# Performance work log

Measured on AMD Instinct MI355X. Metric: run time of the kernel, lower is better.

The kernel has to match this reference:

```python
import jax, jax.numpy as jnp
import numpy as np

IN_F = 256
OUT_F = 256
HYPER = 128
BATCH = 4096


def setup_inputs() -> dict:
    key = jax.random.key(0)
    ks = jax.random.split(key, 9)
    s_in = 1.0 / np.sqrt(IN_F)
    s_h = 1.0 / np.sqrt(HYPER)
    x = jax.random.normal(ks[0], (BATCH, IN_F), dtype=jnp.float32)
    # weight_gen: Linear(in, hyper) -> ReLU -> Linear(hyper, in*out)
    W1g = jax.random.uniform(ks[1], (IN_F, HYPER), jnp.float32, -s_in, s_in)
    b1g = jax.random.uniform(ks[2], (HYPER,), jnp.float32, -s_in, s_in)
    W2g = jax.random.uniform(ks[3], (HYPER, IN_F * OUT_F), jnp.float32, -s_h, s_h)
    b2g = jax.random.uniform(ks[4], (IN_F * OUT_F,), jnp.float32, -s_h, s_h)
    # bias_gen: Linear(in, hyper) -> ReLU -> Linear(hyper, out)
    W1b = jax.random.uniform(ks[5], (IN_F, HYPER), jnp.float32, -s_in, s_in)
    b1b = jax.random.uniform(ks[6], (HYPER,), jnp.float32, -s_in, s_in)
    W2b = jax.random.uniform(ks[7], (HYPER, OUT_F), jnp.float32, -s_h, s_h)
    b2b = jax.random.uniform(ks[8], (OUT_F,), jnp.float32, -s_h, s_h)
    return {"x": x, "W1g": W1g, "b1g": b1g, "W2g": W2g, "b2g": b2g,
            "W1b": W1b, "b1b": b1b, "W2b": W2b, "b2b": b2b}


def reference(x, W1g, b1g, W2g, b2g, W1b, b1b, W2b, b2b):
    B = x.shape[0]
    # generate per-sample weights [B, out, in]
    hg = jax.nn.relu(x @ W1g + b1g)                      # [B, hyper]
    weights = (hg @ W2g + b2g).reshape(B, OUT_F, IN_F)   # [B, out, in]
    # generate per-sample bias [B, out]
    hb = jax.nn.relu(x @ W1b + b1b)                      # [B, hyper]
    bias = hb @ W2b + b2b                                # [B, out]
    # batched matvec: bmm(weights, x[...,None]) + bias
    out = jnp.einsum('boi,bi->bo', weights, x) + bias    # [B, out]
    return out
```

## Files before the change

kernel.cpp:

```cpp
#include <hip/hip_runtime.h>

#define AS1 __attribute__((address_space(1)))
#define AS3 __attribute__((address_space(3)))

typedef short short8 __attribute__((ext_vector_type(8)));
typedef float f32x16 __attribute__((ext_vector_type(16)));
typedef unsigned short ushort4v __attribute__((ext_vector_type(4)));

#define BATCH 4096
#define IN_F 256
#define OUT_F 256
#define HYP 128
#define HX 129
#define KP (HX * IN_F)
#define NBUILD (OUT_F * HX / 8)

__device__ __forceinline__ float bf2f(unsigned short u) {
  unsigned v = ((unsigned)u) << 16;
  float f;
  __builtin_memcpy(&f, &v, 4);
  return f;
}
__device__ __forceinline__ unsigned short f2bf(float f) {
  unsigned u;
  __builtin_memcpy(&u, &f, 4);
  unsigned r = u + 0x7fffu + ((u >> 16) & 1u);
  return (unsigned short)(r >> 16);
}

__device__ __forceinline__ void gld_lds16(const unsigned short* g, unsigned short* s) {
  __builtin_amdgcn_global_load_lds((const AS1 unsigned int*)g, (AS3 unsigned int*)s, 16, 0, 0);
}

__global__ __launch_bounds__(256) void k_prep(
    const float* __restrict__ x,
    const float* __restrict__ W1g, const float* __restrict__ b1g,
    const float* __restrict__ W2g, const float* __restrict__ b2g,
    const float* __restrict__ W1b, const float* __restrict__ b1b,
    const float* __restrict__ W2b, const float* __restrict__ b2b,
    unsigned short* __restrict__ Vb,
    unsigned short* __restrict__ hgbT,
    unsigned short* __restrict__ xb,
    float* __restrict__ out) {
  __shared__ float xl[16 * IN_F];
  __shared__ float hbl[16 * HYP];
  __shared__ unsigned short hgt[HYP * 16];
  const int t = threadIdx.x;

  if (blockIdx.x >= 256) {
    const int cid = (blockIdx.x - 256) * 256 + t;
    const int ic = cid & 31;
    const int pair = cid >> 5;
    const int h = pair % HX;
    const int o = pair / HX;
    const float* src = (h < HYP) ? (W2g + (size_t)h * (OUT_F * IN_F) + o * IN_F + ic * 8)
                                 : (b2g + o * IN_F + ic * 8);
    const float4 v0 = ((const float4*)src)[0];
    const float4 v1 = ((const float4*)src)[1];
    uint4 pk;
    pk.x = (unsigned)f2bf(v0.x) | ((unsigned)f2bf(v0.y) << 16);
    pk.y = (unsigned)f2bf(v0.z) | ((unsigned)f2bf(v0.w) << 16);
    pk.z = (unsigned)f2bf(v1.x) | ((unsigned)f2bf(v1.y) << 16);
    pk.w = (unsigned)f2bf(v1.z) | ((unsigned)f2bf(v1.w) << 16);
    *(uint4*)(Vb + (size_t)o * KP + h * IN_F + ic * 8) = pk;
    return;
  }

  const int r0 = blockIdx.x * 16;
  for (int j0 = 0; j0 < 16 * IN_F; j0 += 256) {
    const float v = x[(size_t)r0 * IN_F + j0 + t];
    xl[j0 + t] = v;
    xb[(size_t)r0 * IN_F + j0 + t] = f2bf(v);
  }
  __syncthreads();
  const int h = t & 127;
  const int rb = (t >> 7) * 8;
  float ag[8] = {0.f, 0.f, 0.f, 0.f, 0.f, 0.f, 0.f, 0.f};
  float av[8] = {0.f, 0.f, 0.f, 0.f, 0.f, 0.f, 0.f, 0.f};
  for (int i = 0; i < IN_F; ++i) {
    const float wg = W1g[i * HYP + h];
    const float wb = W1b[i * HYP + h];
#pragma unroll
    for (int r = 0; r < 8; ++r) {
      const float xv = xl[(rb + r) * IN_F + i];
      ag[r] += xv * wg;
      av[r] += xv * wb;
    }
  }
  const float bg = b1g[h], bb = b1b[h];
#pragma unroll
  for (int r = 0; r < 8; ++r) {
    float g = ag[r] + bg; g = g > 0.f ? g : 0.f;
    float v = av[r] + bb; v = v > 0.f ? v : 0.f;
    hgt[h * 16 + rb + r] = f2bf(g);
    hbl[(rb + r) * HYP + h] = v;
  }
  __syncthreads();
  {
    const int h2 = t >> 1, part = t & 1;
    const uint4 pk = *(const uint4*)&hgt[h2 * 16 + part * 8];
    *(uint4*)&hgbT[(size_t)h2 * BATCH + r0 + part * 8] = pk;
  }
  float acc[16];
#pragma unroll
  for (int r = 0; r < 16; ++r) acc[r] = 0.f;
  for (int hh = 0; hh < HYP; ++hh) {
    const float w = W2b[hh * OUT_F + t];
#pragma unroll
    for (int r = 0; r < 16; ++r) acc[r] += hbl[r * HYP + hh] * w;
  }
  const float bo = b2b[t];
#pragma unroll
  for (int r = 0; r < 16; ++r) out[(size_t)(r0 + r) * OUT_F + t] = acc[r] + bo;
}

__global__ __launch_bounds__(512, 2) void k_gemm(const unsigned short* __restrict__ Vb,
                                                 const unsigned short* __restrict__ hgbT,
                                                 const unsigned short* __restrict__ xb,
                                                 float* __restrict__ out) {
  __shared__ __align__(16) unsigned short Bl[2][64 * 256];
  __shared__ __align__(16) unsigned short hgs[33 * 256];
  const int tid = threadIdx.x;
  const int lane = tid & 63;
  const int wave = tid >> 6;
  const int l31 = lane & 31;
  const int hi = lane >> 5;
  const int wm = wave & 3;
  const int wo = wave >> 2;

  const int bid = blockIdx.x;
  const int c = bid & 7;
  const int t2 = bid >> 3;
  const int xm = t2 & 15;
  const int g8 = t2 >> 4;
  const int grp = c + 8 * g8;
  const int yo = grp & 3;
  const int z = grp >> 2;

  const int m0 = xm * 256;
  const int o0 = yo * 64;
  const int hBeg = (z * HX) >> 2;
  const int hEnd = ((z + 1) * HX) >> 2;
  const int nh = hEnd - hBeg;

  for (int idx = tid; idx < nh * 256; idx += 512) {
    const int hl = idx >> 8;
    const int hh = hBeg + hl;
    hgs[idx] = (hh == HYP) ? (unsigned short)0x3F80
                           : hgbT[(size_t)hh * BATCH + m0 + (idx & 255)];
  }

  const int mrow0 = m0 + wm * 64 + l31;
  const int mrow1 = mrow0 + 32;
  uint4 xf0[16], xf1[16];
#pragma unroll
  for (int j = 0; j < 16; ++j) {
    xf0[j] = *(const uint4*)(xb + (size_t)mrow0 * IN_F + j * 16 + hi * 8);
    xf1[j] = *(const uint4*)(xb + (size_t)mrow1 * IN_F + j * 16 + hi * 8);
  }

  const int nB = tid >> 5;
  const int p = tid & 31;
  const int cs = p ^ (nB & 7);
  const unsigned short* gsrc = Vb + (size_t)(o0 + nB) * KP + cs * 8 + (size_t)hBeg * IN_F;

  f32x16 zv;
#pragma unroll
  for (int i = 0; i < 16; ++i) zv[i] = 0.0f;
  f32x16 acc0 = zv, acc1 = zv;
  f32x16 ah0 = zv, ah1 = zv;

#pragma unroll
  for (int j = 0; j < 4; ++j)
    gld_lds16(gsrc + (size_t)j * 16 * KP, &Bl[0][(tid + 512 * j) * 8]);
  __syncthreads();

  for (int r = 0; r < nh; ++r) {
    const int buf = r & 1;
    if (r + 1 < nh) {
      const unsigned short* gs = gsrc + (size_t)(r + 1) * IN_F;
#pragma unroll
      for (int j = 0; j < 4; ++j)
        gld_lds16(gs + (size_t)j * 16 * KP, &Bl[buf ^ 1][(tid + 512 * j) * 8]);
    }
    const unsigned short* bp = &Bl[buf][0];
    const int rowb = wo * 32 + l31;
#pragma unroll
    for (int ic = 0; ic < 4; ++ic) {
#pragma unroll
      for (int t = 0; t < 4; ++t) {
        const int c0 = ic * 8 + t * 2 + hi;
        const int pr = c0 ^ (l31 & 7);
        const short8 b0 = *(const short8*)(bp + rowb * 256 + pr * 8);
        const short8 a0 = __builtin_bit_cast(short8, xf0[ic * 4 + t]);
        const short8 a1 = __builtin_bit_cast(short8, xf1[ic * 4 + t]);
        ah0 = __builtin_amdgcn_mfma_f32_32x32x16_bf16(a0, b0, ah0, 0, 0, 0);
        ah1 = __builtin_amdgcn_mfma_f32_32x32x16_bf16(a1, b0, ah1, 0, 0, 0);
      }
    }
#pragma unroll
    for (int q = 0; q < 4; ++q) {
      const ushort4v v0 = *(const ushort4v*)&hgs[r * 256 + wm * 64 + 4 * hi + q * 8];
      const ushort4v v1 = *(const ushort4v*)&hgs[r * 256 + wm * 64 + 32 + 4 * hi + q * 8];
#pragma unroll
      for (int e = 0; e < 4; ++e) {
        acc0[q * 4 + e] += bf2f(v0[e]) * ah0[q * 4 + e];
        acc1[q * 4 + e] += bf2f(v1[e]) * ah1[q * 4 + e];
      }
    }
    ah0 = zv; ah1 = zv;
    __syncthreads();
  }

  const int mb = m0 + wm * 64 + 4 * hi;
  const int col = o0 + wo * 32 + l31;
#pragma unroll
  for (int g = 0; g < 16; ++g) {
    const int row0 = mb + (g & 3) + 8 * (g >> 2);
    atomicAdd(&out[(size_t)row0 * OUT_F + col], acc0[g]);
    atomicAdd(&out[(size_t)(row0 + 32) * OUT_F + col], acc1[g]);
  }
}

extern "C" void kernel_launch(void* const* d_in, const int* in_sizes, int n_in,
                              void* d_out, int out_size, void* d_ws, size_t ws_size,
                              hipStream_t stream) {
  const float* x = (const float*)d_in[0];
  const float* W1g = (const float*)d_in[1];
  const float* b1g = (const float*)d_in[2];
  const float* W2g = (const float*)d_in[3];
  const float* b2g = (const float*)d_in[4];
  const float* W1b = (const float*)d_in[5];
  const float* b1b = (const float*)d_in[6];
  const float* W2b = (const float*)d_in[7];
  const float* b2b = (const float*)d_in[8];
  float* out = (float*)d_out;

  char* ws = (char*)d_ws;
  const size_t szV = (size_t)OUT_F * KP * 2;
  const size_t szHg = (size_t)HYP * BATCH * 2;
  unsigned short* Vb = (unsigned short*)ws;
  unsigned short* hgbT = (unsigned short*)(ws + szV);
  unsigned short* xb = (unsigned short*)(ws + szV + szHg);

  hipLaunchKernelGGL(k_prep, dim3(256 + NBUILD), dim3(256), 0, stream,
                     x, W1g, b1g, W2g, b2g, W1b, b1b, W2b, b2b, Vb, hgbT, xb, out);
  hipLaunchKernelGGL(k_gemm, dim3(256), dim3(512), 0, stream,
                     Vb, hgbT, xb, out);
}
```

Measured before the change: 200.4 us.

## Move hypernetwork first and bias layers onto bf16 MFMA with pre-transposed weights

Replaces the scalar FP32 loops in the prep kernel, which compute the hidden activations and the bias-generator output, with bf16 32x32x16 MFMA tiles over 128-row blocks. A new small kernel first transposes W1g/W1b/W2b into bf16. The W2g-to-Vb conversion blocks are coarsened to 512 threads with 4 chunks each. This lowers bias and hidden precision to bf16 and adds a third launch.

Result: faster. 186.2 us (-7.1%).

```diff
diff --git a/kernel.cpp b/kernel.cpp
--- a/kernel.cpp
+++ b/kernel.cpp
@@ -13,7 +13,8 @@
 #define HYP 128
 #define HX 129
 #define KP (HX * IN_F)
-#define NBUILD (OUT_F * HX / 8)
+#define NGEMMP 32
+#define NVB 516
 
 __device__ __forceinline__ float bf2f(unsigned short u) {
   unsigned v = ((unsigned)u) << 16;
@@ -32,86 +33,181 @@
   __builtin_amdgcn_global_load_lds((const AS1 unsigned int*)g, (AS3 unsigned int*)s, 16, 0, 0);
 }
 
-__global__ __launch_bounds__(256) void k_prep(
+__global__ __launch_bounds__(256) void k_trans(const float* __restrict__ W1g,
+                                               const float* __restrict__ W1b,
+                                               const float* __restrict__ W2b,
+                                               unsigned short* __restrict__ W1T,
+                                               unsigned short* __restrict__ W2bT) {
+  const int t = threadIdx.x, b = blockIdx.x;
+  if (b < 64) {
+#pragma unroll
+    for (int i = 0; i < 4; ++i) {
+      const int e = b * 1024 + i * 256 + t;
+      const int n = e >> 8, k = e & 255;
+      const float v = (n < HYP) ? W1g[k * HYP + n] : W1b[k * HYP + (n - HYP)];
+      W1T[e] = f2bf(v);
+    }
+  } else {
+#pragma unroll
+    for (int i = 0; i < 4; ++i) {
+      const int e = (b - 64) * 1024 + i * 256 + t;
+      const int o = e >> 7, h = e & 127;
+      W2bT[e] = f2bf(W2b[h * OUT_F + o]);
+    }
+  }
+}
+
+__global__ __launch_bounds__(512) void k_prep(
     const float* __restrict__ x,
-    const float* __restrict__ W1g, const float* __restrict__ b1g,
+    const float* __restrict__ b1g, const float* __restrict__ b1b,
+    const float* __restrict__ b2b,
     const float* __restrict__ W2g, const float* __restrict__ b2g,
-    const float* __restrict__ W1b, const float* __restrict__ b1b,
-    const float* __restrict__ W2b, const float* __restrict__ b2b,
-    unsigned short* __restrict__ Vb,
-    unsigned short* __restrict__ hgbT,
-    unsigned short* __restrict__ xb,
-    float* __restrict__ out) {
-  __shared__ float xl[16 * IN_F];
-  __shared__ float hbl[16 * HYP];
-  __shared__ unsigned short hgt[HYP * 16];
+    const unsigned short* __restrict__ W1T, const unsigned short* __restrict__ W2bT,
+    unsigned short* __restrict__ Vb, unsigned short* __restrict__ hgbT,
+    unsigned short* __restrict__ xb, float* __restrict__ out) {
+  __shared__ __align__(16) unsigned short xS[128 * 256];
+  __shared__ __align__(16) unsigned short hbS[128 * 128];
   const int t = threadIdx.x;
 
-  if (blockIdx.x >= 256) {
-    const int cid = (blockIdx.x - 256) * 256 + t;
-    const int ic = cid & 31;
-    const int pair = cid >> 5;
-    const int h = pair % HX;
-    const int o = pair / HX;
-    const float* src = (h < HYP) ? (W2g + (size_t)h * (OUT_F * IN_F) + o * IN_F + ic * 8)
-                                 : (b2g + o * IN_F + ic * 8);
-    const float4 v0 = ((const float4*)src)[0];
-    const float4 v1 = ((const float4*)src)[1];
-    uint4 pk;
-    pk.x = (unsigned)f2bf(v0.x) | ((unsigned)f2bf(v0.y) << 16);
-    pk.y = (unsigned)f2bf(v0.z) | ((unsigned)f2bf(v0.w) << 16);
-    pk.z = (unsigned)f2bf(v1.x) | ((unsigned)f2bf(v1.y) << 16);
-    pk.w = (unsigned)f2bf(v1.z) | ((unsigned)f2bf(v1.w) << 16);
-    *(uint4*)(Vb + (size_t)o * KP + h * IN_F + ic * 8) = pk;
+  if (blockIdx.x >= NGEMMP) {
+    const int base = (blockIdx.x - NGEMMP) * 2048 + t;
+#pragma unroll
+    for (int it = 0; it < 4; ++it) {
+      const int cid = base + it * 512;
+      const int ic = cid & 31;
+      const int pair = cid >> 5;
+      const int h = pair % HX;
+      const int o = pair / HX;
+      const float* src = (h < HYP) ? (W2g + (size_t)h * (OUT_F * IN_F) + o * IN_F + ic * 8)
+                                   : (b2g + o * IN_F + ic * 8);
+      const float4 v0 = ((const float4*)src)[0];
+      const float4 v1 = ((const float4*)src)[1];
+      uint4 pk;
+      pk.x = (unsigned)f2bf(v0.x) | ((unsigned)f2bf(v0.y) << 16);
+      pk.y = (unsigned)f2bf(v0.z) | ((unsigned)f2bf(v0.w) << 16);
+      pk.z = (unsigned)f2bf(v1.x) | ((unsigned)f2bf(v1.y) << 16);
+      pk.w = (unsigned)f2bf(v1.z) | ((unsigned)f2bf(v1.w) << 16);
+      *(uint4*)(Vb + (size_t)o * KP + h * IN_F + ic * 8) = pk;
+    }
     return;
   }
 
-  const int r0 = blockIdx.x * 16;
-  for (int j0 = 0; j0 < 16 * IN_F; j0 += 256) {
-    const float v = x[(size_t)r0 * IN_F + j0 + t];
-    xl[j0 + t] = v;
-    xb[(size_t)r0 * IN_F + j0 + t] = f2bf(v);
+  const int lane = t & 63;
+  const int w = t >> 6;
+  const int l31 = lane & 31;
+  const int hi = lane >> 5;
+  const int m0 = blockIdx.x * 128;
+
+#pragma unroll
+  for (int j = 0; j < 16; ++j) {
+    const int row = j * 8 + w;
+    const float4 v = *(const float4*)(x + (size_t)(m0 + row) * IN_F + lane * 4);
+    uint2 pk;
+    pk.x = (unsigned)f2bf(v.x) | ((unsigned)f2bf(v.y) << 16);
+    pk.y = (unsigned)f2bf(v.z) | ((unsigned)f2bf(v.w) << 16);
+    *(uint2*)(xb + (size_t)(m0 + row) * IN_F + lane * 4) = pk;
+    const int ch = lane >> 1, half = lane & 1;
+    *(uint2*)(&xS[row * 256 + ((ch ^ (row & 31))) * 8 + half * 4]) = pk;
   }
   __syncthreads();
-  const int h = t & 127;
-  const int rb = (t >> 7) * 8;
-  float ag[8] = {0.f, 0.f, 0.f, 0.f, 0.f, 0.f, 0.f, 0.f};
-  float av[8] = {0.f, 0.f, 0.f, 0.f, 0.f, 0.f, 0.f, 0.f};
-  for (int i = 0; i < IN_F; ++i) {
-    const float wg = W1g[i * HYP + h];
-    const float wb = W1b[i * HYP + h];
-#pragma unroll
-    for (int r = 0; r < 8; ++r) {
-      const float xv = xl[(rb + r) * IN_F + i];
-      ag[r] += xv * wg;
-      av[r] += xv * wb;
-    }
-  }
-  const float bg = b1g[h], bb = b1b[h];
-#pragma unroll
-  for (int r = 0; r < 8; ++r) {
-    float g = ag[r] + bg; g = g > 0.f ? g : 0.f;
-    float v = av[r] + bb; v = v > 0.f ? v : 0.f;
-    hgt[h * 16 + rb + r] = f2bf(g);
-    hbl[(rb + r) * HYP + h] = v;
+
+  const int hA = w * 32 + l31;
+  uint4 af[16];
+#pragma unroll
+  for (int kt = 0; kt < 16; ++kt)
+    af[kt] = *(const uint4*)(W1T + (size_t)hA * 256 + kt * 16 + hi * 8);
+
+  f32x16 zv;
+#pragma unroll
+  for (int i = 0; i < 16; ++i) zv[i] = 0.0f;
+  f32x16 d0 = zv, d1 = zv, d2 = zv, d3 = zv;
+#pragma unroll
+  for (int kt = 0; kt < 16; ++kt) {
+    const int pos = (kt * 2 + hi) ^ l31;
+    const short8 a = __builtin_bit_cast(short8, af[kt]);
+#define G1STEP(CS, DD)                                                        \
+    {                                                                         \
+      const short8 bfrg = *(const short8*)(&xS[(CS * 32 + l31) * 256 + pos * 8]); \
+      DD = __builtin_amdgcn_mfma_f32_32x32x16_bf16(a, bfrg, DD, 0, 0, 0);     \
+    }
+    G1STEP(0, d0) G1STEP(1, d1) G1STEP(2, d2) G1STEP(3, d3)
+#undef G1STEP
+  }
+
+  if (w < 4) {
+    float4 bq[4];
+#pragma unroll
+    for (int q = 0; q < 4; ++q)
+      bq[q] = *(const float4*)(b1g + w * 32 + q * 8 + hi * 4);
+#define EPI_G(CS, DD)                                                         \
+    {                                                                         \
+      const int mcol = m0 + CS * 32 + l31;                                    \
+      _Pragma("unroll")                                                       \
+      for (int g = 0; g < 16; ++g) {                                          \
+        const int h = w * 32 + (g & 3) + 8 * (g >> 2) + 4 * hi;               \
+        float v = DD[g] + ((const float*)&bq[g >> 2])[g & 3];                 \
+        v = v > 0.f ? v : 0.f;                                                \
+        hgbT[(size_t)h * BATCH + mcol] = f2bf(v);                             \
+      }                                                                       \
+    }
+    EPI_G(0, d0) EPI_G(1, d1) EPI_G(2, d2) EPI_G(3, d3)
+#undef EPI_G
+  } else {
+    float4 bq[4];
+#pragma unroll
+    for (int q = 0; q < 4; ++q)
+      bq[q] = *(const float4*)(b1b + (w - 4) * 32 + q * 8 + hi * 4);
+#define EPI_B(CS, DD)                                                         \
+    {                                                                         \
+      const int m = CS * 32 + l31;                                            \
+      _Pragma("unroll")                                                       \
+      for (int q = 0; q < 4; ++q) {                                           \
+        float v0 = DD[q * 4 + 0] + ((const float*)&bq[q])[0];                 \
+        float v1 = DD[q * 4 + 1] + ((const float*)&bq[q])[1];                 \
+        float v2 = DD[q * 4 + 2] + ((const float*)&bq[q])[2];                 \
+        float v3 = DD[q * 4 + 3] + ((const float*)&bq[q])[3];                 \
+        v0 = v0 > 0.f ? v0 : 0.f; v1 = v1 > 0.f ? v1 : 0.f;                   \
+        v2 = v2 > 0.f ? v2 : 0.f; v3 = v3 > 0.f ? v3 : 0.f;                   \
+        uint2 pk;                                                             \
+        pk.x = (unsigned)f2bf(v0) | ((unsigned)f2bf(v1) << 16);               \
+        pk.y = (unsigned)f2bf(v2) | ((unsigned)f2bf(v3) << 16);               \
+        const int chunk = (w - 4) * 4 + q;                                    \
+        *(uint2*)(&hbS[m * 128 + ((chunk ^ (m & 15))) * 8 + hi * 4]) = pk;    \
+      }                                                                       \
+    }
+    EPI_B(0, d0) EPI_B(1, d1) EPI_B(2, d2) EPI_B(3, d3)
+#undef EPI_B
   }
   __syncthreads();
-  {
-    const int h2 = t >> 1, part = t & 1;
-    const uint4 pk = *(const uint4*)&hgt[h2 * 16 + part * 8];
-    *(uint4*)&hgbT[(size_t)h2 * BATCH + r0 + part * 8] = pk;
-  }
-  float acc[16];
-#pragma unroll
-  for (int r = 0; r < 16; ++r) acc[r] = 0.f;
-  for (int hh = 0; hh < HYP; ++hh) {
-    const float w = W2b[hh * OUT_F + t];
-#pragma unroll
-    for (int r = 0; r < 16; ++r) acc[r] += hbl[r * HYP + hh] * w;
-  }
-  const float bo = b2b[t];
-#pragma unroll
-  for (int r = 0; r < 16; ++r) out[(size_t)(r0 + r) * OUT_F + t] = acc[r] + bo;
+
+  const int msub = w & 3, oh = w >> 2;
+  const int mA = msub * 32 + l31;
+  f32x16 e0 = zv, e1 = zv, e2 = zv, e3 = zv;
+#pragma unroll
+  for (int kt = 0; kt < 8; ++kt) {
+    const int pos = (kt * 2 + hi) ^ (mA & 15);
+    const short8 a = *(const short8*)(&hbS[mA * 128 + pos * 8]);
+#define G2STEP(OS, EE)                                                        \
+    {                                                                         \
+      const int orow = oh * 128 + OS * 32 + l31;                              \
+      const short8 bb = *(const short8*)(W2bT + (size_t)orow * 128 + kt * 16 + hi * 8); \
+      EE = __builtin_amdgcn_mfma_f32_32x32x16_bf16(a, bb, EE, 0, 0, 0);       \
+    }
+    G2STEP(0, e0) G2STEP(1, e1) G2STEP(2, e2) G2STEP(3, e3)
+#undef G2STEP
+  }
+#define EPI2(OS, EE)                                                          \
+  {                                                                           \
+    const int o = oh * 128 + OS * 32 + l31;                                   \
+    const float bo = b2b[o];                                                  \
+    _Pragma("unroll")                                                         \
+    for (int g = 0; g < 16; ++g) {                                            \
+      const int m = m0 + msub * 32 + (g & 3) + 8 * (g >> 2) + 4 * hi;         \
+      out[(size_t)m * OUT_F + o] = EE[g] + bo;                                \
+    }                                                                         \
+  }
+  EPI2(0, e0) EPI2(1, e1) EPI2(2, e2) EPI2(3, e3)
+#undef EPI2
 }
 
 __global__ __launch_bounds__(512, 2) void k_gemm(const unsigned short* __restrict__ Vb,
@@ -239,12 +335,16 @@
   char* ws = (char*)d_ws;
   const size_t szV = (size_t)OUT_F * KP * 2;
   const size_t szHg = (size_t)HYP * BATCH * 2;
+  const size_t szXb = (size_t)BATCH * IN_F * 2;
+  const size_t szW1T = (size_t)256 * 256 * 2;
   unsigned short* Vb = (unsigned short*)ws;
   unsigned short* hgbT = (unsigned short*)(ws + szV);
   unsigned short* xb = (unsigned short*)(ws + szV + szHg);
-
-  hipLaunchKernelGGL(k_prep, dim3(256 + NBUILD), dim3(256), 0, stream,
-                     x, W1g, b1g, W2g, b2g, W1b, b1b, W2b, b2b, Vb, hgbT, xb, out);
-  hipLaunchKernelGGL(k_gemm, dim3(256), dim3(512), 0, stream,
-                     Vb, hgbT, xb, out);
-}
+  unsigned short* W1T = (unsigned short*)(ws + szV + szHg + szXb);
+  unsigned short* W2bT = (unsigned short*)(ws + szV + szHg + szXb + szW1T);
+
+  hipLaunchKernelGGL(k_trans, dim3(96), dim3(256), 0, stream, W1g, W1b, W2b, W1T, W2bT);
+  hipLaunchKernelGGL(k_prep, dim3(NGEMMP + NVB), dim3(512), 0, stream,
+                     x, b1g, b1b, b2b, W2g, b2g, W1T, W2bT, Vb, hgbT, xb, out);
+  hipLaunchKernelGGL(k_gemm, dim3(256), dim3(512), 0, stream, Vb, hgbT, xb, out);
+}
```
